# Optimization experiments

Measured on AMD Instinct MI355X. Metric: run time of the kernel, lower is better.

The kernel has to match this reference:

```python
import jax, jax.numpy as jnp
import numpy as np

N = 50000      # nodes
E = 800000     # edges (before self loops)
IN = 256       # input feature dim
H = 4          # heads
C = 64         # hidden per head (concat=False -> mean over heads -> 64)
LAT = 32       # latent dim
ED = 3         # edge feature dim
NEG_SLOPE = 0.2


def setup_inputs() -> dict:
    key = jax.random.key(0)
    ks = jax.random.split(key, 24)
    nrm = lambda k, shp, s=0.05: jax.random.normal(k, shp, jnp.float32) * s
    inp = {
        'x': jax.random.normal(ks[0], (N, IN), jnp.float32),
        'edge_index': jax.random.randint(ks[1], (2, E), 0, N),
        'edge_attr': jax.random.normal(ks[2], (E, ED), jnp.float32),
    }
    i = 3
    for l, d in enumerate([IN, C]):  # layer 0 in_dim=IN, layer 1 in_dim=hidden
        inp[f'Wl{l}'] = nrm(ks[i], (d, H * C)); i += 1
        inp[f'bl{l}'] = jnp.zeros((H * C,), jnp.float32)
        inp[f'Wr{l}'] = nrm(ks[i], (d, H * C)); i += 1
        inp[f'br{l}'] = jnp.zeros((H * C,), jnp.float32)
        inp[f'We{l}'] = nrm(ks[i], (ED, H * C)); i += 1
        inp[f'att{l}'] = nrm(ks[i], (H, C)); i += 1
        inp[f'bias{l}'] = jnp.zeros((C,), jnp.float32)
    inp['Wmu'] = nrm(ks[i], (C, LAT)); i += 1
    inp['bmu'] = jnp.zeros((LAT,), jnp.float32)
    return inp


def _gatv2(x, edge_index, edge_attr, Wl, bl, Wr, br, We, att, bias):
    # PyG GATv2Conv: heads=H, concat=False, add_self_loops=True,
    # edge_dim=3, fill_value='mean', negative_slope=0.2, share_weights=False
    n = x.shape[0]
    src, dst = edge_index[0], edge_index[1]
    # self-loop edge_attr = mean of incoming edge_attr per node (0 if none)
    deg = jax.ops.segment_sum(jnp.ones((src.shape[0],), jnp.float32), dst, num_segments=n)
    loop_attr = jax.ops.segment_sum(edge_attr, dst, num_segments=n) / jnp.maximum(deg, 1.0)[:, None]
    loop = jnp.arange(n)
    s = jnp.concatenate([src, loop])
    d = jnp.concatenate([dst, loop])
    ea = jnp.concatenate([edge_attr, loop_attr], axis=0)
    xl = (x @ Wl + bl).reshape(n, H, C)   # source transform
    xr = (x @ Wr + br).reshape(n, H, C)   # target transform
    ee = (ea @ We).reshape(-1, H, C)      # edge transform (no bias)
    m = jax.nn.leaky_relu(xl[s] + xr[d] + ee, NEG_SLOPE)   # [Etot, H, C]
    alpha = jnp.einsum('ehc,hc->eh', m, att)                # [Etot, H]
    amax = jax.ops.segment_max(alpha, d, num_segments=n)    # per-dst max (all segments nonempty: self loops)
    ex = jnp.exp(alpha - amax[d])
    a = ex / jax.ops.segment_sum(ex, d, num_segments=n)[d]  # segment softmax
    out = jax.ops.segment_sum(xl[s] * a[:, :, None], d, num_segments=n)  # [N, H, C]
    return out.mean(axis=1) + bias  # concat=False -> head mean, then bias


def reference(x, edge_index, edge_attr,
              Wl0, bl0, Wr0, br0, We0, att0, bias0,
              Wl1, bl1, Wr1, br1, We1, att1, bias1,
              Wmu, bmu):
    h = jax.nn.relu(_gatv2(x, edge_index, edge_attr, Wl0, bl0, Wr0, br0, We0, att0, bias0))
    h = jax.nn.relu(_gatv2(h, edge_index, edge_attr, Wl1, bl1, Wr1, br1, We1, att1, bias1))
    return h @ Wmu + bmu
```

## Files before the change

kernel.cpp:

```cpp
#include <hip/hip_runtime.h>


#define NN  50000
#define EE  800000
#define HC  256
#define NSLOPE 0.2f

typedef float f32x4 __attribute__((ext_vector_type(4)));
typedef short bf16x8 __attribute__((ext_vector_type(8)));

__device__ __forceinline__ unsigned short f2b(float f) {
    unsigned u = __float_as_uint(f);
    u += 0x7FFFu + ((u >> 16) & 1u);
    return (unsigned short)(u >> 16);
}
__device__ __forceinline__ float b2f(unsigned short h) {
    return __uint_as_float((unsigned)h << 16);
}

__global__ __launch_bounds__(256) void deg_kernel(
    const int* __restrict__ dst, int* __restrict__ deg)
{
    int i = blockIdx.x * 256 + threadIdx.x;
    if (i >= EE / 4) return;
    int4 v = ((const int4*)dst)[i];
    atomicAdd(&deg[v.x], 1);
    atomicAdd(&deg[v.y], 1);
    atomicAdd(&deg[v.z], 1);
    atomicAdd(&deg[v.w], 1);
}

__global__ __launch_bounds__(1024) void scan_kernel(
    const int* __restrict__ deg, int* __restrict__ row_start, int* __restrict__ cursor)
{
    __shared__ int sums[1024];
    const int tid = threadIdx.x;
    const int CH = (NN + 1023) / 1024;
    int b = tid * CH, e = min(b + CH, NN);
    int s = 0;
    for (int i = b; i < e; i++) s += deg[i];
    sums[tid] = s;
    __syncthreads();
    for (int off = 1; off < 1024; off <<= 1) {
        int v = (tid >= off) ? sums[tid - off] : 0;
        __syncthreads();
        sums[tid] += v;
        __syncthreads();
    }
    int run = (tid == 0) ? 0 : sums[tid - 1];
    for (int i = b; i < e; i++) {
        row_start[i] = run;
        cursor[i]    = run;
        run += deg[i];
    }
    if (tid == 0) row_start[NN] = EE;
}

__global__ __launch_bounds__(256) void scatter_kernel(
    const int* __restrict__ ei, const float* __restrict__ ea,
    int* __restrict__ cursor, float4* __restrict__ csr)
{
    int i = blockIdx.x * 256 + threadIdx.x;
    if (i >= EE / 4) return;
    int4 s = ((const int4*)ei)[i];
    int4 d = ((const int4*)(ei + EE))[i];
    float4 e0 = ((const float4*)ea)[i * 3 + 0];
    float4 e1 = ((const float4*)ea)[i * 3 + 1];
    float4 e2 = ((const float4*)ea)[i * 3 + 2];
    int p0 = atomicAdd(&cursor[d.x], 1);
    int p1 = atomicAdd(&cursor[d.y], 1);
    int p2 = atomicAdd(&cursor[d.z], 1);
    int p3 = atomicAdd(&cursor[d.w], 1);
    csr[p0] = make_float4(__int_as_float(s.x), e0.x, e0.y, e0.z);
    csr[p1] = make_float4(__int_as_float(s.y), e0.w, e1.x, e1.y);
    csr[p2] = make_float4(__int_as_float(s.z), e1.z, e1.w, e2.x);
    csr[p3] = make_float4(__int_as_float(s.w), e2.y, e2.z, e2.w);
}

__global__ __launch_bounds__(256) void cvt_wt(
    const float* __restrict__ W, unsigned short* __restrict__ WTh,
    unsigned short* __restrict__ WTl, int K)
{
    int i = blockIdx.x * 256 + threadIdx.x;
    if (i >= K * 256) return;
    int k = i >> 8, c = i & 255;
    float v = W[i];
    unsigned short h = f2b(v);
    unsigned short l = f2b(v - b2f(h));
    WTh[(size_t)c * K + k] = h;
    WTl[(size_t)c * K + k] = l;
}

__global__ __launch_bounds__(256) void gemm_mfma(
    const float* __restrict__ A,
    const unsigned short* __restrict__ BTh, const unsigned short* __restrict__ BTl,
    const float* __restrict__ bias, float* __restrict__ C,
    int M, int K)
{
    __shared__ unsigned short Ah[64][40], Al[64][40];
    __shared__ unsigned short Bh[128][40], Bl[128][40];
    const int tid = threadIdx.x;
    const int bm = blockIdx.y << 6;
    const int bn = blockIdx.x << 7;
    const int w  = tid >> 6, l = tid & 63;
    const int wr = w >> 1, wc = w & 1;
    const int lr = l & 15, lk = l >> 4;

    f32x4 acc[2][4];
#pragma unroll
    for (int a = 0; a < 2; a++)
#pragma unroll
        for (int b = 0; b < 4; b++) acc[a][b] = (f32x4){0.f, 0.f, 0.f, 0.f};

    const int ar = tid >> 2, ac = (tid & 3) << 3;

    for (int k0 = 0; k0 < K; k0 += 32) {
        float av[8];
        if (bm + ar < M) {
            *(float4*)&av[0] = *(const float4*)&A[(size_t)(bm + ar) * K + k0 + ac];
            *(float4*)&av[4] = *(const float4*)&A[(size_t)(bm + ar) * K + k0 + ac + 4];
        } else {
#pragma unroll
            for (int j = 0; j < 8; j++) av[j] = 0.f;
        }
        unsigned hp[4], lp[4];
#pragma unroll
        for (int j = 0; j < 4; j++) {
            unsigned short h0 = f2b(av[2 * j]),     h1 = f2b(av[2 * j + 1]);
            unsigned short l0 = f2b(av[2 * j]     - b2f(h0));
            unsigned short l1 = f2b(av[2 * j + 1] - b2f(h1));
            hp[j] = (unsigned)h0 | ((unsigned)h1 << 16);
            lp[j] = (unsigned)l0 | ((unsigned)l1 << 16);
        }
        *(uint4*)&Ah[ar][ac] = make_uint4(hp[0], hp[1], hp[2], hp[3]);
        *(uint4*)&Al[ar][ac] = make_uint4(lp[0], lp[1], lp[2], lp[3]);
#pragma unroll
        for (int rep = 0; rep < 2; rep++) {
            int idx = tid + (rep << 8);
            int rb = idx >> 2, cb = (idx & 3) << 3;
            *(uint4*)&Bh[rb][cb] = *(const uint4*)&BTh[(size_t)(bn + rb) * K + k0 + cb];
            *(uint4*)&Bl[rb][cb] = *(const uint4*)&BTl[(size_t)(bn + rb) * K + k0 + cb];
        }
        __syncthreads();

        bf16x8 afh[2], afl[2], bfh[4], bfl[4];
#pragma unroll
        for (int a = 0; a < 2; a++) {
            afh[a] = *(const bf16x8*)&Ah[wr * 32 + a * 16 + lr][lk << 3];
            afl[a] = *(const bf16x8*)&Al[wr * 32 + a * 16 + lr][lk << 3];
        }
#pragma unroll
        for (int b = 0; b < 4; b++) {
            bfh[b] = *(const bf16x8*)&Bh[wc * 64 + b * 16 + lr][lk << 3];
            bfl[b] = *(const bf16x8*)&Bl[wc * 64 + b * 16 + lr][lk << 3];
        }
#pragma unroll
        for (int a = 0; a < 2; a++)
#pragma unroll
            for (int b = 0; b < 4; b++) {
                acc[a][b] = __builtin_amdgcn_mfma_f32_16x16x32_bf16(afh[a], bfh[b], acc[a][b], 0, 0, 0);
                acc[a][b] = __builtin_amdgcn_mfma_f32_16x16x32_bf16(afh[a], bfl[b], acc[a][b], 0, 0, 0);
                acc[a][b] = __builtin_amdgcn_mfma_f32_16x16x32_bf16(afl[a], bfh[b], acc[a][b], 0, 0, 0);
            }
        __syncthreads();
    }

#pragma unroll
    for (int a = 0; a < 2; a++) {
        int rbase = bm + wr * 32 + a * 16 + (lk << 2);
#pragma unroll
        for (int b = 0; b < 4; b++) {
            int cg = bn + wc * 64 + b * 16 + lr;
            float bs = bias[cg];
#pragma unroll
            for (int i = 0; i < 4; i++) {
                int rg = rbase + i;
                if (rg < M) C[(size_t)rg * HC + cg] = acc[a][b][i] + bs;
            }
        }
    }
}

__global__ __launch_bounds__(256) void gat_edge(
    const float* __restrict__ xl, const float* __restrict__ xr,
    const float4* __restrict__ csr, const int* __restrict__ row_start,
    const float* __restrict__ att, const float* __restrict__ We,
    const float* __restrict__ bias, float* __restrict__ out)
{
    const int lane = threadIdx.x & 63;
    const int node = (blockIdx.x * 256 + threadIdx.x) >> 6;
    if (node >= NN) return;
    const int j4 = lane << 2;
    const float4* xlv = (const float4*)xl;

    const float4 xr4 = *(const float4*)&xr[(size_t)node * HC + j4];
    const float4 at4 = *(const float4*)&att[j4];
    const float4 w0  = *(const float4*)&We[j4];
    const float4 w1  = *(const float4*)&We[HC + j4];
    const float4 w2  = *(const float4*)&We[2 * HC + j4];

    float acc0 = 0.f, acc1 = 0.f, acc2 = 0.f, acc3 = 0.f, denom = 0.f;
    float eas0 = 0.f, eas1 = 0.f, eas2 = 0.f;
    const int beg = row_start[node];
    const int n   = row_start[node + 1] - beg;
    const float4* cp = csr + beg;

    float4 r0 = {0,0,0,0}, r1 = {0,0,0,0}, r2 = {0,0,0,0};
    float4 v0 = {0,0,0,0}, v1 = {0,0,0,0};
    if (n > 0) { r0 = cp[0]; v0 = xlv[(size_t)__float_as_int(r0.x) * 64 + lane]; }
    if (n > 1) { r1 = cp[1]; v1 = xlv[(size_t)__float_as_int(r1.x) * 64 + lane]; }
    if (n > 2) { r2 = cp[2]; }

    for (int i = 0; i < n; i++) {
        float4 crec = r0, cxv = v0;
        r0 = r1; r1 = r2; v0 = v1;
        if (i + 3 < n) r2 = cp[i + 3];
        if (i + 2 < n) v1 = xlv[(size_t)__float_as_int(r1.x) * 64 + lane];

        float ea0 = crec.y, ea1 = crec.z, ea2 = crec.w;
        eas0 += ea0; eas1 += ea1; eas2 += ea2;
        float m0 = cxv.x + xr4.x + ea0 * w0.x + ea1 * w1.x + ea2 * w2.x;
        float m1 = cxv.y + xr4.y + ea0 * w0.y + ea1 * w1.y + ea2 * w2.y;
        float m2 = cxv.z + xr4.z + ea0 * w0.z + ea1 * w1.z + ea2 * w2.z;
        float m3 = cxv.w + xr4.w + ea0 * w0.w + ea1 * w1.w + ea2 * w2.w;
        m0 = fmaxf(m0, NSLOPE * m0);
        m1 = fmaxf(m1, NSLOPE * m1);
        m2 = fmaxf(m2, NSLOPE * m2);
        m3 = fmaxf(m3, NSLOPE * m3);
        float p = m0 * at4.x + m1 * at4.y + m2 * at4.z + m3 * at4.w;
        p += __shfl_xor(p, 1);
        p += __shfl_xor(p, 2);
        p += __shfl_xor(p, 4);
        p += __shfl_xor(p, 8);
        float ex = __expf(p);
        denom += ex;
        acc0 = fmaf(ex, cxv.x, acc0);
        acc1 = fmaf(ex, cxv.y, acc1);
        acc2 = fmaf(ex, cxv.z, acc2);
        acc3 = fmaf(ex, cxv.w, acc3);
    }

    {
        float rd = 1.0f / fmaxf((float)n, 1.0f);
        float ea0 = eas0 * rd, ea1 = eas1 * rd, ea2 = eas2 * rd;
        float4 sv = xlv[(size_t)node * 64 + lane];
        float m0 = sv.x + xr4.x + ea0 * w0.x + ea1 * w1.x + ea2 * w2.x;
        float m1 = sv.y + xr4.y + ea0 * w0.y + ea1 * w1.y + ea2 * w2.y;
        float m2 = sv.z + xr4.z + ea0 * w0.z + ea1 * w1.z + ea2 * w2.z;
        float m3 = sv.w + xr4.w + ea0 * w0.w + ea1 * w1.w + ea2 * w2.w;
        m0 = fmaxf(m0, NSLOPE * m0);
        m1 = fmaxf(m1, NSLOPE * m1);
        m2 = fmaxf(m2, NSLOPE * m2);
        m3 = fmaxf(m3, NSLOPE * m3);
        float p = m0 * at4.x + m1 * at4.y + m2 * at4.z + m3 * at4.w;
        p += __shfl_xor(p, 1);
        p += __shfl_xor(p, 2);
        p += __shfl_xor(p, 4);
        p += __shfl_xor(p, 8);
        float ex = __expf(p);
        denom += ex;
        acc0 = fmaf(ex, sv.x, acc0);
        acc1 = fmaf(ex, sv.y, acc1);
        acc2 = fmaf(ex, sv.z, acc2);
        acc3 = fmaf(ex, sv.w, acc3);
    }

    const float inv = 1.0f / denom;
    float r0s = acc0 * inv, r1s = acc1 * inv, r2s = acc2 * inv, r3s = acc3 * inv;
    r0s += __shfl_xor(r0s, 16); r0s += __shfl_xor(r0s, 32);
    r1s += __shfl_xor(r1s, 16); r1s += __shfl_xor(r1s, 32);
    r2s += __shfl_xor(r2s, 16); r2s += __shfl_xor(r2s, 32);
    r3s += __shfl_xor(r3s, 16); r3s += __shfl_xor(r3s, 32);
    if (lane < 16) {
        float4 bv = *(const float4*)&bias[j4];
        float4 o;
        o.x = fmaxf(0.25f * r0s + bv.x, 0.f);
        o.y = fmaxf(0.25f * r1s + bv.y, 0.f);
        o.z = fmaxf(0.25f * r2s + bv.z, 0.f);
        o.w = fmaxf(0.25f * r3s + bv.w, 0.f);
        *(float4*)&out[(size_t)node * 64 + j4] = o;
    }
}

__global__ __launch_bounds__(256) void mu_kernel(
    const float* __restrict__ h, const float* __restrict__ Wmu,
    const float* __restrict__ bmu, float* __restrict__ out)
{
    __shared__ float ws[64 * 32];
    __shared__ float hs[8 * 64];
    const int tid = threadIdx.x;
#pragma unroll
    for (int i = 0; i < 8; i++) ws[tid + i * 256] = Wmu[tid + i * 256];
    const int nb = blockIdx.x * 8;
    {
        int idx = tid * 2;
        *(float2*)&hs[idx] = *(const float2*)&h[(size_t)nb * 64 + idx];
    }
    __syncthreads();
    const int ln = tid >> 5;
    const int o  = tid & 31;
    float acc = bmu[o];
#pragma unroll
    for (int k = 0; k < 64; k++) acc = fmaf(hs[ln * 64 + k], ws[k * 32 + o], acc);
    out[(size_t)(nb + ln) * 32 + o] = acc;
}

extern "C" void kernel_launch(void* const* d_in, const int* in_sizes, int n_in,
                              void* d_out, int out_size, void* d_ws, size_t ws_size,
                              hipStream_t stream) {
    const float* x    = (const float*)d_in[0];
    const int*   ei   = (const int*)  d_in[1];
    const float* ea   = (const float*)d_in[2];
    const float* Wl0  = (const float*)d_in[3];
    const float* bl0  = (const float*)d_in[4];
    const float* Wr0  = (const float*)d_in[5];
    const float* br0  = (const float*)d_in[6];
    const float* We0  = (const float*)d_in[7];
    const float* att0 = (const float*)d_in[8];
    const float* bi0  = (const float*)d_in[9];
    const float* Wl1  = (const float*)d_in[10];
    const float* bl1  = (const float*)d_in[11];
    const float* Wr1  = (const float*)d_in[12];
    const float* br1  = (const float*)d_in[13];
    const float* We1  = (const float*)d_in[14];
    const float* att1 = (const float*)d_in[15];
    const float* bi1  = (const float*)d_in[16];
    const float* Wmu  = (const float*)d_in[17];
    const float* bmu  = (const float*)d_in[18];
    float* out = (float*)d_out;

    float* xl32 = (float*)d_ws;
    float* xr32 = xl32 + (size_t)NN * HC;
    float* h1   = xr32 + (size_t)NN * HC;
    int*   deg  = (int*)(h1 + (size_t)NN * 64);
    int*   rows = deg + NN;
    int*   curs = rows + NN + 1;
    uintptr_t p = (uintptr_t)(curs + NN);
    p = (p + 15) & ~(uintptr_t)15;
    unsigned short* wt = (unsigned short*)p;
    unsigned short* Wl0Th = wt;                  unsigned short* Wl0Tl = wt + 65536;
    unsigned short* Wr0Th = wt + 65536 * 2;      unsigned short* Wr0Tl = wt + 65536 * 3;
    unsigned short* Wl1Th = wt + 65536 * 4;      unsigned short* Wl1Tl = Wl1Th + 16384;
    unsigned short* Wr1Th = Wl1Th + 16384 * 2;   unsigned short* Wr1Tl = Wl1Th + 16384 * 3;
    p = (uintptr_t)(Wl1Th + 16384 * 4);
    p = (p + 255) & ~(uintptr_t)255;
    float4* csr = (float4*)p;

    hipMemsetAsync(deg, 0, NN * sizeof(int), stream);
    deg_kernel<<<(EE / 4 + 255) / 256, 256, 0, stream>>>(ei + EE, deg);
    scan_kernel<<<1, 1024, 0, stream>>>(deg, rows, curs);
    scatter_kernel<<<(EE / 4 + 255) / 256, 256, 0, stream>>>(ei, ea, curs, csr);

    cvt_wt<<<256, 256, 0, stream>>>(Wl0, Wl0Th, Wl0Tl, 256);
    cvt_wt<<<256, 256, 0, stream>>>(Wr0, Wr0Th, Wr0Tl, 256);
    cvt_wt<<< 64, 256, 0, stream>>>(Wl1, Wl1Th, Wl1Tl, 64);
    cvt_wt<<< 64, 256, 0, stream>>>(Wr1, Wr1Th, Wr1Tl, 64);

    dim3 gg(2, (NN + 63) / 64);
    const int gat_grid = (NN * 64) / 256;

    gemm_mfma<<<gg, 256, 0, stream>>>(x, Wl0Th, Wl0Tl, bl0, xl32, NN, 256);
    gemm_mfma<<<gg, 256, 0, stream>>>(x, Wr0Th, Wr0Tl, br0, xr32, NN, 256);
    gat_edge<<<gat_grid, 256, 0, stream>>>(xl32, xr32, csr, rows, att0, We0, bi0, h1);

    gemm_mfma<<<gg, 256, 0, stream>>>(h1, Wl1Th, Wl1Tl, bl1, xl32, NN, 64);
    gemm_mfma<<<gg, 256, 0, stream>>>(h1, Wr1Th, Wr1Tl, br1, xr32, NN, 64);
    gat_edge<<<gat_grid, 256, 0, stream>>>(xl32, xr32, csr, rows, att1, We1, bi1, h1);

    mu_kernel<<<NN / 8, 256, 0, stream>>>(h1, Wmu, bmu, out);
}
```

Baseline: 721.3 us.

## Fuse left/right projection GEMMs and process four nodes per wave in GAT edge kernel

The two GEMMs per layer (source and target transforms) are merged into one launch over a concatenated 512-column weight. Each block now computes a 64x256 tile, so the A operand is loaded and split into bf16 hi/lo parts once per column tile instead of twice per layer. The LDS row padding changes from 40 to 36. The edge aggregation kernel now has each wavefront loop over four consecutive nodes, cutting the grid by four and amortizing the per-wave weight loads. In exchange, accumulator register pressure doubles in the GEMM, and fewer waves are available to hide gather latency in the edge kernel.

```diff
diff --git a/kernel.cpp b/kernel.cpp
--- a/kernel.cpp
+++ b/kernel.cpp
@@ -91,26 +91,27 @@
     WTl[(size_t)c * K + k] = l;
 }
 
-__global__ __launch_bounds__(256) void gemm_mfma(
+__global__ __launch_bounds__(256) void gemm_fused(
     const float* __restrict__ A,
     const unsigned short* __restrict__ BTh, const unsigned short* __restrict__ BTl,
-    const float* __restrict__ bias, float* __restrict__ C,
+    const float* __restrict__ bias0, const float* __restrict__ bias1,
+    float* __restrict__ C0, float* __restrict__ C1,
     int M, int K)
 {
-    __shared__ unsigned short Ah[64][40], Al[64][40];
-    __shared__ unsigned short Bh[128][40], Bl[128][40];
+    __shared__ unsigned short Ah[64][36], Al[64][36];
+    __shared__ unsigned short Bh[256][36], Bl[256][36];
     const int tid = threadIdx.x;
     const int bm = blockIdx.y << 6;
-    const int bn = blockIdx.x << 7;
+    const int bn = blockIdx.x << 8;
     const int w  = tid >> 6, l = tid & 63;
     const int wr = w >> 1, wc = w & 1;
     const int lr = l & 15, lk = l >> 4;
 
-    f32x4 acc[2][4];
+    f32x4 acc[2][8];
 #pragma unroll
     for (int a = 0; a < 2; a++)
 #pragma unroll
-        for (int b = 0; b < 4; b++) acc[a][b] = (f32x4){0.f, 0.f, 0.f, 0.f};
+        for (int b = 0; b < 8; b++) acc[a][b] = (f32x4){0.f, 0.f, 0.f, 0.f};
 
     const int ar = tid >> 2, ac = (tid & 3) << 3;
 
@@ -135,47 +136,47 @@
         *(uint4*)&Ah[ar][ac] = make_uint4(hp[0], hp[1], hp[2], hp[3]);
         *(uint4*)&Al[ar][ac] = make_uint4(lp[0], lp[1], lp[2], lp[3]);
 #pragma unroll
-        for (int rep = 0; rep < 2; rep++) {
-            int idx = tid + (rep << 8);
-            int rb = idx >> 2, cb = (idx & 3) << 3;
+        for (int rep = 0; rep < 4; rep++) {
+            int i  = (rep << 8) + tid;
+            int rb = i >> 2, cb = (i & 3) << 3;
             *(uint4*)&Bh[rb][cb] = *(const uint4*)&BTh[(size_t)(bn + rb) * K + k0 + cb];
             *(uint4*)&Bl[rb][cb] = *(const uint4*)&BTl[(size_t)(bn + rb) * K + k0 + cb];
         }
         __syncthreads();
 
-        bf16x8 afh[2], afl[2], bfh[4], bfl[4];
+        bf16x8 afh[2], afl[2];
 #pragma unroll
         for (int a = 0; a < 2; a++) {
             afh[a] = *(const bf16x8*)&Ah[wr * 32 + a * 16 + lr][lk << 3];
             afl[a] = *(const bf16x8*)&Al[wr * 32 + a * 16 + lr][lk << 3];
         }
 #pragma unroll
-        for (int b = 0; b < 4; b++) {
-            bfh[b] = *(const bf16x8*)&Bh[wc * 64 + b * 16 + lr][lk << 3];
-            bfl[b] = *(const bf16x8*)&Bl[wc * 64 + b * 16 + lr][lk << 3];
-        }
-#pragma unroll
-        for (int a = 0; a < 2; a++)
-#pragma unroll
-            for (int b = 0; b < 4; b++) {
-                acc[a][b] = __builtin_amdgcn_mfma_f32_16x16x32_bf16(afh[a], bfh[b], acc[a][b], 0, 0, 0);
-                acc[a][b] = __builtin_amdgcn_mfma_f32_16x16x32_bf16(afh[a], bfl[b], acc[a][b], 0, 0, 0);
-                acc[a][b] = __builtin_amdgcn_mfma_f32_16x16x32_bf16(afl[a], bfh[b], acc[a][b], 0, 0, 0);
+        for (int b = 0; b < 8; b++) {
+            bf16x8 bh = *(const bf16x8*)&Bh[wc * 128 + b * 16 + lr][lk << 3];
+            bf16x8 bl_ = *(const bf16x8*)&Bl[wc * 128 + b * 16 + lr][lk << 3];
+#pragma unroll
+            for (int a = 0; a < 2; a++) {
+                acc[a][b] = __builtin_amdgcn_mfma_f32_16x16x32_bf16(afh[a], bh,  acc[a][b], 0, 0, 0);
+                acc[a][b] = __builtin_amdgcn_mfma_f32_16x16x32_bf16(afh[a], bl_, acc[a][b], 0, 0, 0);
+                acc[a][b] = __builtin_amdgcn_mfma_f32_16x16x32_bf16(afl[a], bh,  acc[a][b], 0, 0, 0);
             }
+        }
         __syncthreads();
     }
 
+    const float* bias = (bn == 0) ? bias0 : bias1;
+    float* C = (bn == 0) ? C0 : C1;
 #pragma unroll
     for (int a = 0; a < 2; a++) {
         int rbase = bm + wr * 32 + a * 16 + (lk << 2);
 #pragma unroll
-        for (int b = 0; b < 4; b++) {
-            int cg = bn + wc * 64 + b * 16 + lr;
-            float bs = bias[cg];
+        for (int b = 0; b < 8; b++) {
+            int c = wc * 128 + b * 16 + lr;
+            float bs = bias[c];
 #pragma unroll
             for (int i = 0; i < 4; i++) {
                 int rg = rbase + i;
-                if (rg < M) C[(size_t)rg * HC + cg] = acc[a][b][i] + bs;
+                if (rg < M) C[(size_t)rg * HC + c] = acc[a][b][i] + bs;
             }
         }
     }
@@ -188,97 +189,102 @@
     const float* __restrict__ bias, float* __restrict__ out)
 {
     const int lane = threadIdx.x & 63;
-    const int node = (blockIdx.x * 256 + threadIdx.x) >> 6;
-    if (node >= NN) return;
+    const int wid  = (blockIdx.x * 256 + threadIdx.x) >> 6;
+    const int base = wid << 2;
     const int j4 = lane << 2;
     const float4* xlv = (const float4*)xl;
 
-    const float4 xr4 = *(const float4*)&xr[(size_t)node * HC + j4];
     const float4 at4 = *(const float4*)&att[j4];
     const float4 w0  = *(const float4*)&We[j4];
     const float4 w1  = *(const float4*)&We[HC + j4];
     const float4 w2  = *(const float4*)&We[2 * HC + j4];
 
-    float acc0 = 0.f, acc1 = 0.f, acc2 = 0.f, acc3 = 0.f, denom = 0.f;
-    float eas0 = 0.f, eas1 = 0.f, eas2 = 0.f;
-    const int beg = row_start[node];
-    const int n   = row_start[node + 1] - beg;
-    const float4* cp = csr + beg;
-
-    float4 r0 = {0,0,0,0}, r1 = {0,0,0,0}, r2 = {0,0,0,0};
-    float4 v0 = {0,0,0,0}, v1 = {0,0,0,0};
-    if (n > 0) { r0 = cp[0]; v0 = xlv[(size_t)__float_as_int(r0.x) * 64 + lane]; }
-    if (n > 1) { r1 = cp[1]; v1 = xlv[(size_t)__float_as_int(r1.x) * 64 + lane]; }
-    if (n > 2) { r2 = cp[2]; }
-
-    for (int i = 0; i < n; i++) {
-        float4 crec = r0, cxv = v0;
-        r0 = r1; r1 = r2; v0 = v1;
-        if (i + 3 < n) r2 = cp[i + 3];
-        if (i + 2 < n) v1 = xlv[(size_t)__float_as_int(r1.x) * 64 + lane];
-
-        float ea0 = crec.y, ea1 = crec.z, ea2 = crec.w;
-        eas0 += ea0; eas1 += ea1; eas2 += ea2;
-        float m0 = cxv.x + xr4.x + ea0 * w0.x + ea1 * w1.x + ea2 * w2.x;
-        float m1 = cxv.y + xr4.y + ea0 * w0.y + ea1 * w1.y + ea2 * w2.y;
-        float m2 = cxv.z + xr4.z + ea0 * w0.z + ea1 * w1.z + ea2 * w2.z;
-        float m3 = cxv.w + xr4.w + ea0 * w0.w + ea1 * w1.w + ea2 * w2.w;
-        m0 = fmaxf(m0, NSLOPE * m0);
-        m1 = fmaxf(m1, NSLOPE * m1);
-        m2 = fmaxf(m2, NSLOPE * m2);
-        m3 = fmaxf(m3, NSLOPE * m3);
-        float p = m0 * at4.x + m1 * at4.y + m2 * at4.z + m3 * at4.w;
-        p += __shfl_xor(p, 1);
-        p += __shfl_xor(p, 2);
-        p += __shfl_xor(p, 4);
-        p += __shfl_xor(p, 8);
-        float ex = __expf(p);
-        denom += ex;
-        acc0 = fmaf(ex, cxv.x, acc0);
-        acc1 = fmaf(ex, cxv.y, acc1);
-        acc2 = fmaf(ex, cxv.z, acc2);
-        acc3 = fmaf(ex, cxv.w, acc3);
-    }
-
-    {
-        float rd = 1.0f / fmaxf((float)n, 1.0f);
-        float ea0 = eas0 * rd, ea1 = eas1 * rd, ea2 = eas2 * rd;
-        float4 sv = xlv[(size_t)node * 64 + lane];
-        float m0 = sv.x + xr4.x + ea0 * w0.x + ea1 * w1.x + ea2 * w2.x;
-        float m1 = sv.y + xr4.y + ea0 * w0.y + ea1 * w1.y + ea2 * w2.y;
-        float m2 = sv.z + xr4.z + ea0 * w0.z + ea1 * w1.z + ea2 * w2.z;
-        float m3 = sv.w + xr4.w + ea0 * w0.w + ea1 * w1.w + ea2 * w2.w;
-        m0 = fmaxf(m0, NSLOPE * m0);
-        m1 = fmaxf(m1, NSLOPE * m1);
-        m2 = fmaxf(m2, NSLOPE * m2);
-        m3 = fmaxf(m3, NSLOPE * m3);
-        float p = m0 * at4.x + m1 * at4.y + m2 * at4.z + m3 * at4.w;
-        p += __shfl_xor(p, 1);
-        p += __shfl_xor(p, 2);
-        p += __shfl_xor(p, 4);
-        p += __shfl_xor(p, 8);
-        float ex = __expf(p);
-        denom += ex;
-        acc0 = fmaf(ex, sv.x, acc0);
-        acc1 = fmaf(ex, sv.y, acc1);
-        acc2 = fmaf(ex, sv.z, acc2);
-        acc3 = fmaf(ex, sv.w, acc3);
-    }
-
-    const float inv = 1.0f / denom;
-    float r0s = acc0 * inv, r1s = acc1 * inv, r2s = acc2 * inv, r3s = acc3 * inv;
-    r0s += __shfl_xor(r0s, 16); r0s += __shfl_xor(r0s, 32);
-    r1s += __shfl_xor(r1s, 16); r1s += __shfl_xor(r1s, 32);
-    r2s += __shfl_xor(r2s, 16); r2s += __shfl_xor(r2s, 32);
-    r3s += __shfl_xor(r3s, 16); r3s += __shfl_xor(r3s, 32);
-    if (lane < 16) {
-        float4 bv = *(const float4*)&bias[j4];
-        float4 o;
-        o.x = fmaxf(0.25f * r0s + bv.x, 0.f);
-        o.y = fmaxf(0.25f * r1s + bv.y, 0.f);
-        o.z = fmaxf(0.25f * r2s + bv.z, 0.f);
-        o.w = fmaxf(0.25f * r3s + bv.w, 0.f);
-        *(float4*)&out[(size_t)node * 64 + j4] = o;
+#pragma unroll 1
+    for (int v = 0; v < 4; v++) {
+        const int node = base + v;
+        const float4 xr4 = *(const float4*)&xr[(size_t)node * HC + j4];
+
+        float acc0 = 0.f, acc1 = 0.f, acc2 = 0.f, acc3 = 0.f, denom = 0.f;
+        float eas0 = 0.f, eas1 = 0.f, eas2 = 0.f;
+        const int beg = row_start[node];
+        const int n   = row_start[node + 1] - beg;
+        const float4* cp = csr + beg;
+
+        float4 r0 = {0,0,0,0}, r1 = {0,0,0,0}, r2 = {0,0,0,0};
+        float4 v0 = {0,0,0,0}, v1 = {0,0,0,0};
+        if (n > 0) { r0 = cp[0]; v0 = xlv[(size_t)__float_as_int(r0.x) * 64 + lane]; }
+        if (n > 1) { r1 = cp[1]; v1 = xlv[(size_t)__float_as_int(r1.x) * 64 + lane]; }
+        if (n > 2) { r2 = cp[2]; }
+
+        for (int i = 0; i < n; i++) {
+            float4 crec = r0, cxv = v0;
+            r0 = r1; r1 = r2; v0 = v1;
+            if (i + 3 < n) r2 = cp[i + 3];
+            if (i + 2 < n) v1 = xlv[(size_t)__float_as_int(r1.x) * 64 + lane];
+
+            float ea0 = crec.y, ea1 = crec.z, ea2 = crec.w;
+            eas0 += ea0; eas1 += ea1; eas2 += ea2;
+            float m0 = cxv.x + xr4.x + ea0 * w0.x + ea1 * w1.x + ea2 * w2.x;
+            float m1 = cxv.y + xr4.y + ea0 * w0.y + ea1 * w1.y + ea2 * w2.y;
+            float m2 = cxv.z + xr4.z + ea0 * w0.z + ea1 * w1.z + ea2 * w2.z;
+            float m3 = cxv.w + xr4.w + ea0 * w0.w + ea1 * w1.w + ea2 * w2.w;
+            m0 = fmaxf(m0, NSLOPE * m0);
+            m1 = fmaxf(m1, NSLOPE * m1);
+            m2 = fmaxf(m2, NSLOPE * m2);
+            m3 = fmaxf(m3, NSLOPE * m3);
+            float p = m0 * at4.x + m1 * at4.y + m2 * at4.z + m3 * at4.w;
+            p += __shfl_xor(p, 1);
+            p += __shfl_xor(p, 2);
+            p += __shfl_xor(p, 4);
+            p += __shfl_xor(p, 8);
+            float ex = __expf(p);
+            denom += ex;
+            acc0 = fmaf(ex, cxv.x, acc0);
+            acc1 = fmaf(ex, cxv.y, acc1);
+            acc2 = fmaf(ex, cxv.z, acc2);
+            acc3 = fmaf(ex, cxv.w, acc3);
+        }
+
+        {
+            float rd = 1.0f / fmaxf((float)n, 1.0f);
+            float ea0 = eas0 * rd, ea1 = eas1 * rd, ea2 = eas2 * rd;
+            float4 sv = xlv[(size_t)node * 64 + lane];
+            float m0 = sv.x + xr4.x + ea0 * w0.x + ea1 * w1.x + ea2 * w2.x;
+            float m1 = sv.y + xr4.y + ea0 * w0.y + ea1 * w1.y + ea2 * w2.y;
+            float m2 = sv.z + xr4.z + ea0 * w0.z + ea1 * w1.z + ea2 * w2.z;
+            float m3 = sv.w + xr4.w + ea0 * w0.w + ea1 * w1.w + ea2 * w2.w;
+            m0 = fmaxf(m0, NSLOPE * m0);
+            m1 = fmaxf(m1, NSLOPE * m1);
+            m2 = fmaxf(m2, NSLOPE * m2);
+            m3 = fmaxf(m3, NSLOPE * m3);
+            float p = m0 * at4.x + m1 * at4.y + m2 * at4.z + m3 * at4.w;
+            p += __shfl_xor(p, 1);
+            p += __shfl_xor(p, 2);
+            p += __shfl_xor(p, 4);
+            p += __shfl_xor(p, 8);
+            float ex = __expf(p);
+            denom += ex;
+            acc0 = fmaf(ex, sv.x, acc0);
+            acc1 = fmaf(ex, sv.y, acc1);
+            acc2 = fmaf(ex, sv.z, acc2);
+            acc3 = fmaf(ex, sv.w, acc3);
+        }
+
+        const float inv = 1.0f / denom;
+        float r0s = acc0 * inv, r1s = acc1 * inv, r2s = acc2 * inv, r3s = acc3 * inv;
+        r0s += __shfl_xor(r0s, 16); r0s += __shfl_xor(r0s, 32);
+        r1s += __shfl_xor(r1s, 16); r1s += __shfl_xor(r1s, 32);
+        r2s += __shfl_xor(r2s, 16); r2s += __shfl_xor(r2s, 32);
+        r3s += __shfl_xor(r3s, 16); r3s += __shfl_xor(r3s, 32);
+        if (lane < 16) {
+            float4 bv = *(const float4*)&bias[j4];
+            float4 o;
+            o.x = fmaxf(0.25f * r0s + bv.x, 0.f);
+            o.y = fmaxf(0.25f * r1s + bv.y, 0.f);
+            o.z = fmaxf(0.25f * r2s + bv.z, 0.f);
+            o.w = fmaxf(0.25f * r3s + bv.w, 0.f);
+            *(float4*)&out[(size_t)node * 64 + j4] = o;
+        }
     }
 }
 
@@ -337,12 +343,11 @@
     int*   curs = rows + NN + 1;
     uintptr_t p = (uintptr_t)(curs + NN);
     p = (p + 15) & ~(uintptr_t)15;
-    unsigned short* wt = (unsigned short*)p;
-    unsigned short* Wl0Th = wt;                  unsigned short* Wl0Tl = wt + 65536;
-    unsigned short* Wr0Th = wt + 65536 * 2;      unsigned short* Wr0Tl = wt + 65536 * 3;
-    unsigned short* Wl1Th = wt + 65536 * 4;      unsigned short* Wl1Tl = Wl1Th + 16384;
-    unsigned short* Wr1Th = Wl1Th + 16384 * 2;   unsigned short* Wr1Tl = Wl1Th + 16384 * 3;
-    p = (uintptr_t)(Wl1Th + 16384 * 4);
+    unsigned short* WT0h = (unsigned short*)p;
+    unsigned short* WT0l = WT0h + 512 * 256;
+    unsigned short* WT1h = WT0l + 512 * 256;
+    unsigned short* WT1l = WT1h + 512 * 64;
+    p = (uintptr_t)(WT1l + 512 * 64);
     p = (p + 255) & ~(uintptr_t)255;
     float4* csr = (float4*)p;
 
@@ -351,20 +356,18 @@
     scan_kernel<<<1, 1024, 0, stream>>>(deg, rows, curs);
     scatter_kernel<<<(EE / 4 + 255) / 256, 256, 0, stream>>>(ei, ea, curs, csr);
 
-    cvt_wt<<<256, 256, 0, stream>>>(Wl0, Wl0Th, Wl0Tl, 256);
-    cvt_wt<<<256, 256, 0, stream>>>(Wr0, Wr0Th, Wr0Tl, 256);
-    cvt_wt<<< 64, 256, 0, stream>>>(Wl1, Wl1Th, Wl1Tl, 64);
-    cvt_wt<<< 64, 256, 0, stream>>>(Wr1, Wr1Th, Wr1Tl, 64);
+    cvt_wt<<<256, 256, 0, stream>>>(Wl0, WT0h,             WT0l,             256);
+    cvt_wt<<<256, 256, 0, stream>>>(Wr0, WT0h + 256 * 256, WT0l + 256 * 256, 256);
+    cvt_wt<<< 64, 256, 0, stream>>>(Wl1, WT1h,             WT1l,             64);
+    cvt_wt<<< 64, 256, 0, stream>>>(Wr1, WT1h + 256 * 64,  WT1l + 256 * 64,  64);
 
     dim3 gg(2, (NN + 63) / 64);
-    const int gat_grid = (NN * 64) / 256;
-
-    gemm_mfma<<<gg, 256, 0, stream>>>(x, Wl0Th, Wl0Tl, bl0, xl32, NN, 256);
-    gemm_mfma<<<gg, 256, 0, stream>>>(x, Wr0Th, Wr0Tl, br0, xr32, NN, 256);
+    const int gat_grid = NN / 16;
+
+    gemm_fused<<<gg, 256, 0, stream>>>(x, WT0h, WT0l, bl0, br0, xl32, xr32, NN, 256);
     gat_edge<<<gat_grid, 256, 0, stream>>>(xl32, xr32, csr, rows, att0, We0, bi0, h1);
 
-    gemm_mfma<<<gg, 256, 0, stream>>>(h1, Wl1Th, Wl1Tl, bl1, xl32, NN, 64);
-    gemm_mfma<<<gg, 256, 0, stream>>>(h1, Wr1Th, Wr1Tl, br1, xr32, NN, 64);
+    gemm_fused<<<gg, 256, 0, stream>>>(h1, WT1h, WT1l, bl1, br1, xl32, xr32, NN, 64);
     gat_edge<<<gat_grid, 256, 0, stream>>>(xl32, xr32, csr, rows, att1, We1, bi1, h1);
 
     mu_kernel<<<NN / 8, 256, 0, stream>>>(h1, Wmu, bmu, out);
```

Measured after the change: 727.8 us. Within noise of the previous version (+0.9%).
